# Optimization experiments

Measured on AMD Instinct MI355X. Metric: run time of the kernel, lower is better.

The kernel has to match this reference:

```python
import jax, jax.numpy as jnp
import numpy as np

DIM = 768
HEADS = 12
DIM_HEAD = 64
INNER = HEADS * DIM_HEAD  # 768
N = 197  # num_patches + 1
B = 64


def setup_inputs() -> dict:
    key = jax.random.key(0)
    k0, k1, k2, k3, k4 = jax.random.split(key, 5)
    x = jax.random.normal(k0, (B, N, DIM), dtype=jnp.float32)
    # Linear weights stored as [in, out] for x @ W
    W_qkv = jax.random.normal(k1, (DIM, 3 * INNER), dtype=jnp.float32) * (1.0 / np.sqrt(DIM))
    W_out = jax.random.normal(k2, (INNER, DIM), dtype=jnp.float32) * (1.0 / np.sqrt(INNER))
    b_out = jnp.zeros((DIM,), dtype=jnp.float32)
    scale = jnp.full((HEADS,), DIM_HEAD ** -0.5, dtype=jnp.float32)
    return {"x": x, "scale": scale, "W_qkv": W_qkv, "W_out": W_out, "b_out": b_out}


def reference(x, scale, W_qkv, W_out, b_out):
    b, n, _ = x.shape
    qkv = x @ W_qkv  # [b, n, 3*inner]
    q, k, v = jnp.split(qkv, 3, axis=-1)
    def to_heads(t):
        return t.reshape(b, n, HEADS, DIM_HEAD).transpose(0, 2, 1, 3)  # b h n d
    q, k, v = to_heads(q), to_heads(k), to_heads(v)
    # per-head learnable scale applied to raw dot products
    dots = jnp.einsum('bhid,bhjd->bhij', q, k) * scale[None, :, None, None]
    # diagonal self-mask: set dots[i,i] = -inf before softmax
    diag = jnp.eye(n, dtype=bool)[None, None]
    dots = jnp.where(diag, -jnp.inf, dots)
    attn = jax.nn.softmax(dots, axis=-1)
    out = jnp.einsum('bhij,bhjd->bhid', attn, v)
    out = out.transpose(0, 2, 1, 3).reshape(b, n, INNER)
    return out @ W_out + b_out
```

## Files before the change

### kernel.cpp

```cpp
#include <hip/hip_runtime.h>
#include <hip/hip_bf16.h>

typedef __attribute__((ext_vector_type(8))) short short8;
typedef __attribute__((ext_vector_type(4))) float floatx4;

#define MFMA_BF16(a, b, c) __builtin_amdgcn_mfma_f32_16x16x32_bf16((a), (b), (c), 0, 0, 0)

__device__ __forceinline__ unsigned short f2bf(float f) {
    union { float f; unsigned u; } v; v.f = f;
    unsigned r = v.u + 0x7fffu + ((v.u >> 16) & 1u);
    return (unsigned short)(r >> 16);
}

__global__ void cast_f32_to_bf16(const float* __restrict__ src,
                                 unsigned short* __restrict__ dst, int n4) {
    int i = blockIdx.x * blockDim.x + threadIdx.x;
    int stride = gridDim.x * blockDim.x;
    for (; i < n4; i += stride) {
        float4 f = reinterpret_cast<const float4*>(src)[i];
        ushort4 o;
        o.x = f2bf(f.x); o.y = f2bf(f.y); o.z = f2bf(f.z); o.w = f2bf(f.w);
        reinterpret_cast<ushort4*>(dst)[i] = o;
    }
}

__global__ void transpose_cast(const float* __restrict__ src,
                               unsigned short* __restrict__ dst, int R, int C) {
    __shared__ float tile[32][33];
    int c0 = blockIdx.x * 32, r0 = blockIdx.y * 32;
    int tx = threadIdx.x, ty = threadIdx.y;
#pragma unroll
    for (int i = 0; i < 32; i += 8)
        tile[ty + i][tx] = src[(long)(r0 + ty + i) * C + (c0 + tx)];
    __syncthreads();
#pragma unroll
    for (int i = 0; i < 32; i += 8)
        dst[(long)(c0 + ty + i) * R + (r0 + tx)] = f2bf(tile[tx][ty + i]);
}

template <bool OUT_BF16>
__global__ __launch_bounds__(256, 2) void gemm_bt(
    const unsigned short* __restrict__ A,
    const unsigned short* __restrict__ B,
    void* __restrict__ Cout,
    const float* __restrict__ bias,
    int M, int N, int K) {
    const int LDT = 40;
    __shared__ __align__(16) unsigned short Alds[128 * LDT];
    __shared__ __align__(16) unsigned short Blds[128 * LDT];

    int tid = threadIdx.x;
    int lane = tid & 63, wave = tid >> 6;
    int m0 = blockIdx.y * 128, n0 = blockIdx.x * 128;
    int wm = (wave >> 1) * 64, wn = (wave & 1) * 64;

    floatx4 acc[4][4];
#pragma unroll
    for (int mi = 0; mi < 4; mi++)
#pragma unroll
        for (int ni = 0; ni < 4; ni++) acc[mi][ni] = (floatx4){0.f, 0.f, 0.f, 0.f};

    int srow = tid >> 1;
    int shalf = tid & 1;
    int arow = m0 + srow; if (arow >= M) arow = M - 1;
    const unsigned short* aptr = A + (long)arow * K + shalf * 16;
    const unsigned short* bptr = B + (long)(n0 + srow) * K + shalf * 16;
    unsigned short* aw = &Alds[srow * LDT + shalf * 16];
    unsigned short* bw = &Blds[srow * LDT + shalf * 16];

    for (int k0 = 0; k0 < K; k0 += 32) {
        short8 av0 = *reinterpret_cast<const short8*>(aptr + k0);
        short8 av1 = *reinterpret_cast<const short8*>(aptr + k0 + 8);
        short8 bv0 = *reinterpret_cast<const short8*>(bptr + k0);
        short8 bv1 = *reinterpret_cast<const short8*>(bptr + k0 + 8);
        __syncthreads();
        *reinterpret_cast<short8*>(aw) = av0;
        *reinterpret_cast<short8*>(aw + 8) = av1;
        *reinterpret_cast<short8*>(bw) = bv0;
        *reinterpret_cast<short8*>(bw + 8) = bv1;
        __syncthreads();

        short8 af[4], bfr[4];
#pragma unroll
        for (int mi = 0; mi < 4; mi++)
            af[mi] = *reinterpret_cast<const short8*>(
                &Alds[(wm + mi * 16 + (lane & 15)) * LDT + (lane >> 4) * 8]);
#pragma unroll
        for (int ni = 0; ni < 4; ni++)
            bfr[ni] = *reinterpret_cast<const short8*>(
                &Blds[(wn + ni * 16 + (lane & 15)) * LDT + (lane >> 4) * 8]);
#pragma unroll
        for (int mi = 0; mi < 4; mi++)
#pragma unroll
            for (int ni = 0; ni < 4; ni++)
                acc[mi][ni] = MFMA_BF16(af[mi], bfr[ni], acc[mi][ni]);
    }

    if (OUT_BF16) {
        unsigned short* C = (unsigned short*)Cout;
#pragma unroll
        for (int mi = 0; mi < 4; mi++)
#pragma unroll
            for (int rr = 0; rr < 4; rr++) {
                int row = m0 + wm + mi * 16 + (lane >> 4) * 4 + rr;
                if (row < M) {
                    long rbase = (long)row * N + n0 + wn + (lane & 15);
#pragma unroll
                    for (int ni = 0; ni < 4; ni++)
                        C[rbase + ni * 16] = f2bf(acc[mi][ni][rr]);
                }
            }
    } else {
        float* C = (float*)Cout;
        float bv[4];
#pragma unroll
        for (int ni = 0; ni < 4; ni++) bv[ni] = bias[n0 + wn + ni * 16 + (lane & 15)];
#pragma unroll
        for (int mi = 0; mi < 4; mi++)
#pragma unroll
            for (int rr = 0; rr < 4; rr++) {
                int row = m0 + wm + mi * 16 + (lane >> 4) * 4 + rr;
                if (row < M) {
                    long rbase = (long)row * N + n0 + wn + (lane & 15);
#pragma unroll
                    for (int ni = 0; ni < 4; ni++)
                        C[rbase + ni * 16] = acc[mi][ni][rr] + bv[ni];
                }
            }
    }
}

__global__ __launch_bounds__(448, 2) void attn_kernel(
    const unsigned short* __restrict__ qkv,
    const float* __restrict__ scale,
    unsigned short* __restrict__ out) {
    const int N = 197, D3 = 2304;
    int b = blockIdx.x / 12, h = blockIdx.x % 12;
    int tid = threadIdx.x, lane = tid & 63, wave = tid >> 6;

    __shared__ __align__(16) unsigned short Klds[224 * 64];
    __shared__ __align__(16) unsigned short Vlds[64 * 224];
    __shared__ __align__(16) unsigned short Plds[7 * 16 * 32];

    const unsigned short* base = qkv + (long)b * N * D3 + h * 64;

    for (int idx = tid; idx < 224 * 8; idx += 448) {
        int r = idx >> 3, s = idx & 7;
        short8 v = {0, 0, 0, 0, 0, 0, 0, 0};
        if (r < N) v = *reinterpret_cast<const short8*>(base + (long)r * D3 + 768 + s * 8);
        *reinterpret_cast<short8*>(&Klds[r * 64 + (s ^ (r & 7)) * 8]) = v;
    }
    for (int idx = tid; idx < 224 * 8; idx += 448) {
        int j = idx >> 3, sg = idx & 7;
        short8 v = {0, 0, 0, 0, 0, 0, 0, 0};
        if (j < N) v = *reinterpret_cast<const short8*>(base + (long)j * D3 + 1536 + sg * 8);
        int s = j >> 3;
#pragma unroll
        for (int e = 0; e < 8; e++) {
            int d = sg * 8 + e;
            Vlds[d * 224 + (s ^ (d & 3)) * 8 + (j & 7)] = (unsigned short)v[e];
        }
    }
    __syncthreads();

    float sc = scale[h];
    unsigned short* Pw = &Plds[wave * (16 * 32)];

    for (int rtb = 0; rtb < 2; rtb++) {
        int rt = wave + rtb * 7;
        int i0 = rt * 16;
        int qrow = i0 + (lane & 15); if (qrow > N - 1) qrow = N - 1;
        const unsigned short* qp = base + (long)qrow * D3;
        short8 qf[2];
#pragma unroll
        for (int kb = 0; kb < 2; kb++)
            qf[kb] = *reinterpret_cast<const short8*>(qp + kb * 32 + (lane >> 4) * 8);

        floatx4 sf[14];
#pragma unroll
        for (int jt = 0; jt < 14; jt++) sf[jt] = (floatx4){0.f, 0.f, 0.f, 0.f};
#pragma unroll
        for (int jt = 0; jt < 14; jt++) {
#pragma unroll
            for (int kb = 0; kb < 2; kb++) {
                int r = jt * 16 + (lane & 15);
                int slot = kb * 4 + (lane >> 4);
                short8 kf = *reinterpret_cast<const short8*>(
                    &Klds[r * 64 + (slot ^ (r & 7)) * 8]);
                sf[jt] = MFMA_BF16(qf[kb], kf, sf[jt]);
            }
        }

        int rowg[4];
        float mx[4], sm[4];
#pragma unroll
        for (int rr = 0; rr < 4; rr++) { rowg[rr] = i0 + (lane >> 4) * 4 + rr; mx[rr] = -1e30f; }
#pragma unroll
        for (int jt = 0; jt < 14; jt++) {
            int col = jt * 16 + (lane & 15);
#pragma unroll
            for (int rr = 0; rr < 4; rr++) {
                float v = sf[jt][rr] * sc;
                if (col >= N || col == rowg[rr]) v = -1e30f;
                sf[jt][rr] = v;
                mx[rr] = fmaxf(mx[rr], v);
            }
        }
#pragma unroll
        for (int rr = 0; rr < 4; rr++) {
#pragma unroll
            for (int m = 1; m <= 8; m <<= 1)
                mx[rr] = fmaxf(mx[rr], __shfl_xor(mx[rr], m, 64));
            sm[rr] = 0.f;
        }
#pragma unroll
        for (int jt = 0; jt < 14; jt++)
#pragma unroll
            for (int rr = 0; rr < 4; rr++) {
                float p = __expf(sf[jt][rr] - mx[rr]);
                sf[jt][rr] = p;
                sm[rr] += p;
            }
#pragma unroll
        for (int rr = 0; rr < 4; rr++)
#pragma unroll
            for (int m = 1; m <= 8; m <<= 1)
                sm[rr] += __shfl_xor(sm[rr], m, 64);

        floatx4 oacc[4];
#pragma unroll
        for (int dt = 0; dt < 4; dt++) oacc[dt] = (floatx4){0.f, 0.f, 0.f, 0.f};
#pragma unroll
        for (int c = 0; c < 7; c++) {
#pragma unroll
            for (int jh = 0; jh < 2; jh++) {
#pragma unroll
                for (int rr = 0; rr < 4; rr++) {
                    int row = (lane >> 4) * 4 + rr;
                    int jj = jh * 16 + (lane & 15);
                    Pw[row * 32 + ((jj >> 3) ^ (row & 3)) * 8 + (jj & 7)] =
                        f2bf(sf[c * 2 + jh][rr]);
                }
            }
            int prow = lane & 15;
            short8 pa = *reinterpret_cast<const short8*>(
                &Pw[prow * 32 + (((lane >> 4)) ^ (prow & 3)) * 8]);
#pragma unroll
            for (int dt = 0; dt < 4; dt++) {
                int d = dt * 16 + (lane & 15);
                int slot = c * 4 + (lane >> 4);
                short8 vf = *reinterpret_cast<const short8*>(
                    &Vlds[d * 224 + (slot ^ (d & 3)) * 8]);
                oacc[dt] = MFMA_BF16(pa, vf, oacc[dt]);
            }
        }

#pragma unroll
        for (int rr = 0; rr < 4; rr++) {
            int n = rowg[rr];
            if (n < N) {
                float r = 1.f / sm[rr];
                long o = ((long)b * N + n) * 768 + h * 64;
#pragma unroll
                for (int dt = 0; dt < 4; dt++)
                    out[o + dt * 16 + (lane & 15)] = f2bf(oacc[dt][rr] * r);
            }
        }
    }
}

extern "C" void kernel_launch(void* const* d_in, const int* in_sizes, int n_in,
                              void* d_out, int out_size, void* d_ws, size_t ws_size,
                              hipStream_t stream) {
    (void)in_sizes; (void)n_in; (void)out_size; (void)ws_size;
    const float* x     = (const float*)d_in[0];
    const float* scale = (const float*)d_in[1];
    const float* Wqkv  = (const float*)d_in[2];
    const float* Wout  = (const float*)d_in[3];
    const float* bout  = (const float*)d_in[4];
    float* out = (float*)d_out;

    const int M = 12608;
    char* ws = (char*)d_ws;
    unsigned short* x_bf   = (unsigned short*)(ws);
    unsigned short* wqkv_t = (unsigned short*)(ws + 19365888);
    unsigned short* wout_t = (unsigned short*)(ws + 22904832);
    unsigned short* qkv    = (unsigned short*)(ws + 24084480);
    unsigned short* ao     = (unsigned short*)(ws + 82182144);

    cast_f32_to_bf16<<<2048, 256, 0, stream>>>(x, x_bf, (M * 768) / 4);
    transpose_cast<<<dim3(2304 / 32, 768 / 32), dim3(32, 8), 0, stream>>>(Wqkv, wqkv_t, 768, 2304);
    transpose_cast<<<dim3(768 / 32, 768 / 32), dim3(32, 8), 0, stream>>>(Wout, wout_t, 768, 768);
    gemm_bt<true><<<dim3(2304 / 128, 99), 256, 0, stream>>>(x_bf, wqkv_t, qkv, nullptr, M, 2304, 768);
    attn_kernel<<<768, 448, 0, stream>>>(qkv, scale, ao);
    gemm_bt<false><<<dim3(768 / 128, 99), 256, 0, stream>>>(ao, wout_t, out, bout, M, 768, 768);
}
```

Measured before the change: 232.8 us.

## Load GEMM tiles directly global-to-LDS and raise occupancy target

The GEMM main loop now uses the global_load_lds builtin to copy 16-byte chunks straight from global memory into shared memory, replacing the register round-trip. The unpadded LDS layout (stride 32) is required by the direct-load addressing. Launch bounds change from 2 to 4 blocks per SM. This removes VGPR staging and may raise occupancy, but it drops the prefetch-before-sync overlap, risks LDS bank conflicts on fragment reads, and relies on the barrier waiting for the async LDS writes.

```diff
diff --git a/kernel.cpp b/kernel.cpp
--- a/kernel.cpp
+++ b/kernel.cpp
@@ -10,6 +10,12 @@
     union { float f; unsigned u; } v; v.f = f;
     unsigned r = v.u + 0x7fffu + ((v.u >> 16) & 1u);
     return (unsigned short)(r >> 16);
+}
+
+__device__ __forceinline__ void gload16(const unsigned short* g, unsigned short* l) {
+    __builtin_amdgcn_global_load_lds(
+        (const __attribute__((address_space(1))) unsigned int*)g,
+        (__attribute__((address_space(3))) unsigned int*)l, 16, 0, 0);
 }
 
 __global__ void cast_f32_to_bf16(const float* __restrict__ src,
@@ -39,15 +45,14 @@
 }
 
 template <bool OUT_BF16>
-__global__ __launch_bounds__(256, 2) void gemm_bt(
+__global__ __launch_bounds__(256, 4) void gemm_bt(
     const unsigned short* __restrict__ A,
     const unsigned short* __restrict__ B,
     void* __restrict__ Cout,
     const float* __restrict__ bias,
     int M, int N, int K) {
-    const int LDT = 40;
-    __shared__ __align__(16) unsigned short Alds[128 * LDT];
-    __shared__ __align__(16) unsigned short Blds[128 * LDT];
+    __shared__ __align__(16) unsigned short Alds[128 * 32];
+    __shared__ __align__(16) unsigned short Blds[128 * 32];
 
     int tid = threadIdx.x;
     int lane = tid & 63, wave = tid >> 6;
@@ -60,35 +65,36 @@
 #pragma unroll
         for (int ni = 0; ni < 4; ni++) acc[mi][ni] = (floatx4){0.f, 0.f, 0.f, 0.f};
 
-    int srow = tid >> 1;
-    int shalf = tid & 1;
-    int arow = m0 + srow; if (arow >= M) arow = M - 1;
-    const unsigned short* aptr = A + (long)arow * K + shalf * 16;
-    const unsigned short* bptr = B + (long)(n0 + srow) * K + shalf * 16;
-    unsigned short* aw = &Alds[srow * LDT + shalf * 16];
-    unsigned short* bw = &Blds[srow * LDT + shalf * 16];
+    int srow = tid >> 2;
+    int scol = (tid & 3) * 8;
+    int ar0 = m0 + srow;       if (ar0 >= M) ar0 = M - 1;
+    int ar1 = m0 + 64 + srow;  if (ar1 >= M) ar1 = M - 1;
+    const unsigned short* ap0 = A + (long)ar0 * K + scol;
+    const unsigned short* ap1 = A + (long)ar1 * K + scol;
+    const unsigned short* bp0 = B + (long)(n0 + srow) * K + scol;
+    const unsigned short* bp1 = B + (long)(n0 + 64 + srow) * K + scol;
+    unsigned short* la0 = &Alds[srow * 32 + scol];
+    unsigned short* la1 = &Alds[(64 + srow) * 32 + scol];
+    unsigned short* lb0 = &Blds[srow * 32 + scol];
+    unsigned short* lb1 = &Blds[(64 + srow) * 32 + scol];
 
     for (int k0 = 0; k0 < K; k0 += 32) {
-        short8 av0 = *reinterpret_cast<const short8*>(aptr + k0);
-        short8 av1 = *reinterpret_cast<const short8*>(aptr + k0 + 8);
-        short8 bv0 = *reinterpret_cast<const short8*>(bptr + k0);
-        short8 bv1 = *reinterpret_cast<const short8*>(bptr + k0 + 8);
         __syncthreads();
-        *reinterpret_cast<short8*>(aw) = av0;
-        *reinterpret_cast<short8*>(aw + 8) = av1;
-        *reinterpret_cast<short8*>(bw) = bv0;
-        *reinterpret_cast<short8*>(bw + 8) = bv1;
+        gload16(ap0 + k0, la0);
+        gload16(ap1 + k0, la1);
+        gload16(bp0 + k0, lb0);
+        gload16(bp1 + k0, lb1);
         __syncthreads();
 
         short8 af[4], bfr[4];
 #pragma unroll
         for (int mi = 0; mi < 4; mi++)
             af[mi] = *reinterpret_cast<const short8*>(
-                &Alds[(wm + mi * 16 + (lane & 15)) * LDT + (lane >> 4) * 8]);
+                &Alds[(wm + mi * 16 + (lane & 15)) * 32 + (lane >> 4) * 8]);
 #pragma unroll
         for (int ni = 0; ni < 4; ni++)
             bfr[ni] = *reinterpret_cast<const short8*>(
-                &Blds[(wn + ni * 16 + (lane & 15)) * LDT + (lane >> 4) * 8]);
+                &Blds[(wn + ni * 16 + (lane & 15)) * 32 + (lane >> 4) * 8]);
 #pragma unroll
         for (int mi = 0; mi < 4; mi++)
 #pragma unroll
```

After: 219.7 us. -5.6%, faster.
